# Kernel optimization log

Measured on AMD Instinct MI355X. Metric: run time of the kernel, lower is better.

The kernel has to match this reference:

```python
import jax, jax.numpy as jnp
import numpy as np

B, S, D, H = 4, 2048, 1024, 16
HD = D // H  # head_dim = 64


def setup_inputs() -> dict:
    key = jax.random.key(0)
    ks = jax.random.split(key, 9)
    sc = 1.0 / np.sqrt(D)
    return {
        "x": jax.random.normal(ks[0], (B, S, D), dtype=jnp.float32),
        "Wq": jax.random.normal(ks[1], (D, D), dtype=jnp.float32) * sc,
        "bq": jnp.zeros((D,), dtype=jnp.float32),
        "Wk": jax.random.normal(ks[2], (D, D), dtype=jnp.float32) * sc,
        "bk": jnp.zeros((D,), dtype=jnp.float32),
        "Wv": jax.random.normal(ks[3], (D, D), dtype=jnp.float32) * sc,
        "bv": jnp.zeros((D,), dtype=jnp.float32),
        "Wo": jax.random.normal(ks[4], (D, D), dtype=jnp.float32) * sc,
        "bo": jnp.zeros((D,), dtype=jnp.float32),
    }


def reference(x, Wq, bq, Wk, bk, Wv, bv, Wo, bo):
    # QKV projections (torch Linear: x @ W.T + b), reshape to [B, H, S, HD]
    def proj(W, b):
        return (x @ W.T + b).reshape(B, S, H, HD).transpose(0, 2, 1, 3)

    Q, K, V = proj(Wq, bq), proj(Wk, bk), proj(Wv, bv)
    scores = jnp.einsum("bhqd,bhkd->bhqk", Q, K) / jnp.sqrt(jnp.float32(HD))
    attn = jax.nn.softmax(scores, axis=-1)  # dropout is identity at eval
    ctx = jnp.einsum("bhqk,bhkd->bhqd", attn, V)
    ctx = ctx.transpose(0, 2, 1, 3).reshape(B, S, D)
    out = ctx @ Wo.T + bo
    return out, attn
```

## Files before the change

kernel.cpp:

```cpp
#include <hip/hip_runtime.h>
#include <stdint.h>

#define Mm 8192
#define Dd 1024

typedef unsigned short u16;
typedef __attribute__((ext_vector_type(8))) short bf16x8;
typedef __attribute__((ext_vector_type(4))) float f32x4;
typedef __attribute__((ext_vector_type(4))) u16 u16x4;

__device__ __forceinline__ u16 f2bf(float f) {
  union { float f; uint32_t u; } c; c.f = f;
  uint32_t u = c.u;
  return (u16)((u + 0x7fffu + ((u >> 16) & 1u)) >> 16);
}

__device__ __forceinline__ float EXP2(float x) {
#if __has_builtin(__builtin_amdgcn_exp2f)
  return __builtin_amdgcn_exp2f(x);
#else
  return exp2f(x);
#endif
}

__device__ __forceinline__ float LOG2(float x) {
#if __has_builtin(__builtin_amdgcn_logf)
  return __builtin_amdgcn_logf(x);
#else
  return log2f(x);
#endif
}

__device__ __forceinline__ uint32_t cvtpk(float a, float b) {
  uint32_t r;
  asm("v_cvt_pk_bf16_f32 %0, %1, %2" : "=v"(r) : "v"(a), "v"(b));
  return r;
}

__device__ __forceinline__ void gll16(const void* g, void* l) {
  __builtin_amdgcn_global_load_lds((const __attribute__((address_space(1))) void*)g,
                                   (__attribute__((address_space(3))) void*)l, 16, 0, 0);
}

__global__ void cvt_all(const float* __restrict__ x, const float* __restrict__ wq,
                        const float* __restrict__ wk, const float* __restrict__ wv,
                        const float* __restrict__ wo, u16* __restrict__ out) {
  const int xn4 = 2097152, wn4 = 262144;
  const int total = xn4 + 4 * wn4;
  int i = blockIdx.x * blockDim.x + threadIdx.x;
  int stride = gridDim.x * blockDim.x;
  for (; i < total; i += stride) {
    const float* src; int off;
    if (i < xn4) { src = x; off = i; }
    else {
      int j = i - xn4; int wsel = j >> 18; off = j & (wn4 - 1);
      src = (wsel == 0) ? wq : (wsel == 1) ? wk : (wsel == 2) ? wv : wo;
    }
    float4 v = ((const float4*)src)[off];
    u16x4 o;
    o.x = f2bf(v.x); o.y = f2bf(v.y); o.z = f2bf(v.z); o.w = f2bf(v.w);
    ((u16x4*)out)[i] = o;
  }
}

template<int MODE>
__global__ __launch_bounds__(256) void gemm_bt(
    const u16* __restrict__ A, const u16* __restrict__ Bt,
    const float* __restrict__ bias, void* __restrict__ out,
    int M, int N, int K, float scale)
{
  __shared__ u16 As[128 * 32];
  __shared__ u16 Bs[128 * 32];
  int tiles_n = N >> 7;
  int nwg = (M >> 7) * tiles_n;
  int bid = blockIdx.x;
  { int q = nwg >> 3; bid = (bid & 7) * q + (bid >> 3); }
  int tm = bid / tiles_n, tn = bid % tiles_n;
  int tid = threadIdx.x;
  int wid = tid >> 6, lane = tid & 63;
  int wr = wid >> 1, wc = wid & 1;

  f32x4 acc[4][4] = {};

  int a_row = wr * 64 + (lane & 15);
  int b_row = wc * 64 + (lane & 15);
  int frag_k = (lane >> 4) * 8;

  const u16* ga0 = A + (size_t)(tm * 128 + wid * 32 + (lane >> 2)) * K + (lane & 3) * 8;
  const u16* ga1 = ga0 + (size_t)16 * K;
  const u16* gb0 = Bt + (size_t)(tn * 128 + wid * 32 + (lane >> 2)) * K + (lane & 3) * 8;
  const u16* gb1 = gb0 + (size_t)16 * K;
  u16* lA0 = As + wid * 1024;
  u16* lA1 = As + wid * 1024 + 512;
  u16* lB0 = Bs + wid * 1024;
  u16* lB1 = Bs + wid * 1024 + 512;

  for (int kt = 0; kt < K; kt += 32) {
    gll16(ga0 + kt, lA0);
    gll16(ga1 + kt, lA1);
    gll16(gb0 + kt, lB0);
    gll16(gb1 + kt, lB1);
    __syncthreads();
    bf16x8 af[4], bfr[4];
#pragma unroll
    for (int i = 0; i < 4; i++)
      af[i] = *(const bf16x8*)(As + (a_row + i * 16) * 32 + frag_k);
#pragma unroll
    for (int i = 0; i < 4; i++)
      bfr[i] = *(const bf16x8*)(Bs + (b_row + i * 16) * 32 + frag_k);
#pragma unroll
    for (int i = 0; i < 4; i++)
#pragma unroll
      for (int j = 0; j < 4; j++)
        acc[i][j] = __builtin_amdgcn_mfma_f32_16x16x32_bf16(af[i], bfr[j], acc[i][j], 0, 0, 0);
    __syncthreads();
  }

#pragma unroll
  for (int i = 0; i < 4; i++) {
#pragma unroll
    for (int j = 0; j < 4; j++) {
      int col = tn * 128 + wc * 64 + j * 16 + (lane & 15);
      float bv = bias ? bias[col] : 0.f;
      if (MODE == 2) {
        int row0 = tm * 128 + wr * 64 + i * 16 + (lane >> 4) * 4;
        int b_ = row0 >> 11, s0 = row0 & 2047, h = col >> 6, hd = col & 63;
        u16x4 o;
#pragma unroll
        for (int r = 0; r < 4; r++) o[r] = f2bf((acc[i][j][r] + bv) * scale);
        *(u16x4*)&((u16*)out)[((size_t)(b_ * 16 + h) * 64 + hd) * 2048 + s0] = o;
      } else {
#pragma unroll
        for (int r = 0; r < 4; r++) {
          int row = tm * 128 + wr * 64 + i * 16 + (lane >> 4) * 4 + r;
          float v = (acc[i][j][r] + bv) * scale;
          if (MODE == 0) {
            int b_ = row >> 11, s = row & 2047, h = col >> 6, hd = col & 63;
            ((u16*)out)[(((size_t)(b_ * 16 + h) * 2048 + s) << 6) + hd] = f2bf(v);
          } else {
            ((float*)out)[(size_t)row * N + col] = v;
          }
        }
      }
    }
  }
}

__global__ __launch_bounds__(512) void attn_fused(
    const u16* __restrict__ Qb, const u16* __restrict__ Kb,
    const u16* __restrict__ Vtb, float* __restrict__ attn_out,
    u16* __restrict__ ctxb)
{
  __shared__ u16 Ks[4][4096];
  __shared__ u16 Vs[4][4096];
  __shared__ u16 Ps[8192];

  int bid = blockIdx.x;
  int swz = (bid & 7) * 128 + (bid >> 3);
  int bh = swz >> 4, qt = swz & 15;
  int tid = threadIdx.x, w = tid >> 6, lane = tid & 63;
  int g = lane >> 4, l15 = lane & 15;

  const u16* Qg = Qb + ((size_t)bh * 2048 + qt * 128) * 64;
  const u16* Kg = Kb + (size_t)bh * 2048 * 64;
  const u16* Vg = Vtb + (size_t)bh * 64 * 2048;
  float* Ag = attn_out + ((size_t)bh * 2048 + qt * 128) * 2048;

  int qloc = w * 16 + l15;
  bf16x8 aq0 = *(const bf16x8*)(Qg + (size_t)qloc * 64 + g * 8);
  bf16x8 aq1 = *(const bf16x8*)(Qg + (size_t)qloc * 64 + 32 + g * 8);

  int srow = w * 8 + (lane >> 3);
  int schunk = (lane & 7) ^ (lane >> 3);
  const u16* Ksrc = Kg + (size_t)srow * 64 + schunk * 8;
  const u16* Vsrc = Vg + (size_t)srow * 2048 + schunk * 8;

  float ls0 = 0.f, ls1 = 0.f, ls2 = 0.f, ls3 = 0.f;
#pragma unroll
  for (int p = 0; p < 3; p++)
    gll16(Ksrc + (size_t)p * 4096, (char*)Ks[p] + w * 1024);
  for (int it = 0; it < 32; ++it) {
    gll16(Ksrc + (size_t)((it + 3) & 31) * 4096, (char*)Ks[(it + 3) & 3] + w * 1024);
    asm volatile("s_waitcnt vmcnt(3)" ::: "memory");
    __builtin_amdgcn_s_barrier();
    f32x4 s[4] = {};
    const char* Kbase = (const char*)Ks[it & 3];
    __builtin_amdgcn_s_setprio(1);
#pragma unroll
    for (int t = 0; t < 4; t++) {
      int kr = t * 16 + l15;
      int x = (kr & 7) << 4;
      bf16x8 k0 = *(const bf16x8*)(Kbase + kr * 128 + ((g * 16) ^ x));
      bf16x8 k1 = *(const bf16x8*)(Kbase + kr * 128 + ((64 + g * 16) ^ x));
      s[t] = __builtin_amdgcn_mfma_f32_16x16x32_bf16(k0, aq0, s[t], 0, 0, 0);
      s[t] = __builtin_amdgcn_mfma_f32_16x16x32_bf16(k1, aq1, s[t], 0, 0, 0);
    }
    __builtin_amdgcn_s_setprio(0);
#pragma unroll
    for (int r = 0; r < 4; r++) {
      ls0 += EXP2(s[0][r]); ls1 += EXP2(s[1][r]);
      ls2 += EXP2(s[2][r]); ls3 += EXP2(s[3][r]);
    }
    asm volatile("" ::: "memory");
    __builtin_amdgcn_s_barrier();
  }
  float lsum = (ls0 + ls1) + (ls2 + ls3);
  lsum += __shfl_xor(lsum, 16);
  lsum += __shfl_xor(lsum, 32);
  float lr2 = -LOG2(lsum);

  f32x4 ctx[4] = {};
  int xq = (qloc & 7) << 4;
  char* Pb = (char*)Ps + qloc * 128;
#pragma unroll
  for (int p = 0; p < 3; p++) {
    gll16(Ksrc + (size_t)p * 4096, (char*)Ks[p] + w * 1024);
    gll16(Vsrc + (size_t)p * 64,  (char*)Vs[p] + w * 1024);
  }
  for (int it = 0; it < 32; ++it) {
    int nx = (it + 3) & 31;
    gll16(Ksrc + (size_t)nx * 4096, (char*)Ks[(it + 3) & 3] + w * 1024);
    gll16(Vsrc + (size_t)nx * 64,  (char*)Vs[(it + 3) & 3] + w * 1024);
    if (it == 0)      asm volatile("s_waitcnt vmcnt(6)" ::: "memory");
    else if (it == 1) asm volatile("s_waitcnt vmcnt(10)" ::: "memory");
    else if (it == 2) asm volatile("s_waitcnt vmcnt(14)" ::: "memory");
    else              asm volatile("s_waitcnt vmcnt(18)" ::: "memory");
    __builtin_amdgcn_s_barrier();
    f32x4 s[4] = {};
    const char* Kbase = (const char*)Ks[it & 3];
    __builtin_amdgcn_s_setprio(1);
#pragma unroll
    for (int t = 0; t < 4; t++) {
      int kr = t * 16 + l15;
      int x = (kr & 7) << 4;
      bf16x8 k0 = *(const bf16x8*)(Kbase + kr * 128 + ((g * 16) ^ x));
      bf16x8 k1 = *(const bf16x8*)(Kbase + kr * 128 + ((64 + g * 16) ^ x));
      s[t] = __builtin_amdgcn_mfma_f32_16x16x32_bf16(k0, aq0, s[t], 0, 0, 0);
      s[t] = __builtin_amdgcn_mfma_f32_16x16x32_bf16(k1, aq1, s[t], 0, 0, 0);
    }
    __builtin_amdgcn_s_setprio(0);
    float* Arow = Ag + (size_t)qloc * 2048 + it * 64 + g * 4;
#pragma unroll
    for (int t = 0; t < 4; t++) {
      f32x4 p;
#pragma unroll
      for (int r = 0; r < 4; r++) p[r] = EXP2(s[t][r] + lr2);
      __builtin_nontemporal_store(p, (f32x4*)(Arow + t * 16));
      uint2 pk;
      pk.x = cvtpk(p[0], p[1]);
      pk.y = cvtpk(p[2], p[3]);
      *(uint2*)(Pb + ((t * 32 + g * 8) ^ xq)) = pk;
    }
    __builtin_amdgcn_s_setprio(1);
#pragma unroll
    for (int kk = 0; kk < 2; kk++) {
      bf16x8 ap = *(const bf16x8*)(Pb + ((kk * 64 + g * 16) ^ xq));
#pragma unroll
      for (int t = 0; t < 4; t++) {
        int dr = t * 16 + l15;
        bf16x8 bv = *(const bf16x8*)((const char*)Vs[it & 3] + dr * 128 + ((kk * 64 + g * 16) ^ ((dr & 7) << 4)));
        ctx[t] = __builtin_amdgcn_mfma_f32_16x16x32_bf16(ap, bv, ctx[t], 0, 0, 0);
      }
    }
    __builtin_amdgcn_s_setprio(0);
    asm volatile("" ::: "memory");
    __builtin_amdgcn_s_barrier();
  }

  int b_ = bh >> 4, h = bh & 15;
#pragma unroll
  for (int t = 0; t < 4; t++)
#pragma unroll
    for (int r = 0; r < 4; r++) {
      int qg = qt * 128 + w * 16 + g * 4 + r;
      int col = h * 64 + t * 16 + l15;
      ctxb[((size_t)b_ * 2048 + qg) * 1024 + col] = f2bf(ctx[t][r]);
    }
}

extern "C" void kernel_launch(void* const* d_in, const int* in_sizes, int n_in,
                              void* d_out, int out_size, void* d_ws, size_t ws_size,
                              hipStream_t stream) {
  const float* x  = (const float*)d_in[0];
  const float* Wq = (const float*)d_in[1];
  const float* bq = (const float*)d_in[2];
  const float* Wk = (const float*)d_in[3];
  const float* bk = (const float*)d_in[4];
  const float* Wv = (const float*)d_in[5];
  const float* bv = (const float*)d_in[6];
  const float* Wo = (const float*)d_in[7];
  const float* bo = (const float*)d_in[8];

  u16* xb   = (u16*)d_ws;
  u16* Wqb  = xb + (size_t)Mm * Dd;
  u16* Wkb  = Wqb + (size_t)Dd * Dd;
  u16* Wvb  = Wkb + (size_t)Dd * Dd;
  u16* Wob  = Wvb + (size_t)Dd * Dd;
  u16* Qb   = Wob + (size_t)Dd * Dd;
  u16* Kbuf = Qb + (size_t)Mm * Dd;
  u16* Vtb  = Kbuf + (size_t)Mm * Dd;
  u16* ctxb = Vtb + (size_t)Mm * Dd;

  float* out_f = (float*)d_out;
  float* attn_o = out_f + (size_t)Mm * Dd;

  cvt_all<<<2048, 256, 0, stream>>>(x, Wq, Wk, Wv, Wo, xb);

  const float qscale = 0.125f * 1.44269504088896340736f;
  gemm_bt<0><<<512, 256, 0, stream>>>(xb, Wqb, bq, Qb,   Mm, Dd, Dd, qscale);
  gemm_bt<0><<<512, 256, 0, stream>>>(xb, Wkb, bk, Kbuf, Mm, Dd, Dd, 1.0f);
  gemm_bt<2><<<512, 256, 0, stream>>>(xb, Wvb, bv, Vtb,  Mm, Dd, Dd, 1.0f);
  attn_fused<<<1024, 512, 0, stream>>>(Qb, Kbuf, Vtb, attn_o, ctxb);
  gemm_bt<1><<<512, 256, 0, stream>>>(ctxb, Wob, bo, (void*)out_f, Mm, Dd, Dd, 1.0f);
}
```

Before: 453.9 us.

## Fuse QKV projections into one GEMM and process two query tiles per attention block

The three Q/K/V projection GEMMs become one launch over a concatenated N=3072 weight (Wq/Wk/Wv are contiguous in the workspace), with the epilogue routing columns to Q, K or transposed V. The attention kernel now handles two 128-row query tiles per block. The second tile's row-sum pass is folded into the first tile's output pass, so K tiles are reused and the standalone K sweep count drops from four to three. This trades fewer launches and less K traffic for a smaller grid (512 blocks), more registers, and hand-tuned vmcnt waits that risk being wrong.

New measurement: 532.0 us. 1.17x slower.

```diff
diff --git a/kernel.cpp b/kernel.cpp
--- a/kernel.cpp
+++ b/kernel.cpp
@@ -63,11 +63,87 @@
   }
 }
 
-template<int MODE>
-__global__ __launch_bounds__(256) void gemm_bt(
+__global__ __launch_bounds__(256) void gemm_qkv(
+    const u16* __restrict__ A, const u16* __restrict__ Wt,
+    const float* __restrict__ bq, const float* __restrict__ bk, const float* __restrict__ bv,
+    u16* __restrict__ Qo, u16* __restrict__ Ko, u16* __restrict__ Vo, float qscale)
+{
+  __shared__ u16 As[128 * 32];
+  __shared__ u16 Bs[128 * 32];
+  const int K = 1024, tiles_n = 24;
+  int nwg = 64 * 24;
+  int bid = blockIdx.x;
+  { int q = nwg >> 3; bid = (bid & 7) * q + (bid >> 3); }
+  int tm = bid / tiles_n, tn = bid % tiles_n;
+  int tid = threadIdx.x;
+  int wid = tid >> 6, lane = tid & 63;
+  int wr = wid >> 1, wc = wid & 1;
+
+  f32x4 acc[4][4] = {};
+  int a_row = wr * 64 + (lane & 15);
+  int b_row = wc * 64 + (lane & 15);
+  int frag_k = (lane >> 4) * 8;
+
+  const u16* ga0 = A + (size_t)(tm * 128 + wid * 32 + (lane >> 2)) * K + (lane & 3) * 8;
+  const u16* ga1 = ga0 + (size_t)16 * K;
+  const u16* gb0 = Wt + (size_t)(tn * 128 + wid * 32 + (lane >> 2)) * K + (lane & 3) * 8;
+  const u16* gb1 = gb0 + (size_t)16 * K;
+  u16* lA0 = As + wid * 1024;
+  u16* lA1 = As + wid * 1024 + 512;
+  u16* lB0 = Bs + wid * 1024;
+  u16* lB1 = Bs + wid * 1024 + 512;
+
+  for (int kt = 0; kt < K; kt += 32) {
+    gll16(ga0 + kt, lA0);
+    gll16(ga1 + kt, lA1);
+    gll16(gb0 + kt, lB0);
+    gll16(gb1 + kt, lB1);
+    __syncthreads();
+    bf16x8 af[4], bfr[4];
+#pragma unroll
+    for (int i = 0; i < 4; i++)
+      af[i] = *(const bf16x8*)(As + (a_row + i * 16) * 32 + frag_k);
+#pragma unroll
+    for (int i = 0; i < 4; i++)
+      bfr[i] = *(const bf16x8*)(Bs + (b_row + i * 16) * 32 + frag_k);
+#pragma unroll
+    for (int i = 0; i < 4; i++)
+#pragma unroll
+      for (int j = 0; j < 4; j++)
+        acc[i][j] = __builtin_amdgcn_mfma_f32_16x16x32_bf16(af[i], bfr[j], acc[i][j], 0, 0, 0);
+    __syncthreads();
+  }
+
+#pragma unroll
+  for (int i = 0; i < 4; i++) {
+#pragma unroll
+    for (int j = 0; j < 4; j++) {
+      int col = tn * 128 + wc * 64 + j * 16 + (lane & 15);
+      int wsel = col >> 10, c10 = col & 1023;
+      int h = c10 >> 6, hd = c10 & 63;
+      float bvv = (wsel == 0 ? bq : wsel == 1 ? bk : bv)[c10];
+      int row0 = tm * 128 + wr * 64 + i * 16 + (lane >> 4) * 4;
+      int b_ = row0 >> 11, s0 = row0 & 2047;
+      if (wsel == 2) {
+        u16x4 o;
+#pragma unroll
+        for (int r = 0; r < 4; r++) o[r] = f2bf(acc[i][j][r] + bvv);
+        *(u16x4*)&Vo[((size_t)(b_ * 16 + h) * 64 + hd) * 2048 + s0] = o;
+      } else {
+        u16* dst = (wsel == 0) ? Qo : Ko;
+        float sc = (wsel == 0) ? qscale : 1.0f;
+#pragma unroll
+        for (int r = 0; r < 4; r++)
+          dst[(((size_t)(b_ * 16 + h) * 2048 + (s0 + r)) << 6) + hd] = f2bf((acc[i][j][r] + bvv) * sc);
+      }
+    }
+  }
+}
+
+__global__ __launch_bounds__(256) void gemm_out(
     const u16* __restrict__ A, const u16* __restrict__ Bt,
-    const float* __restrict__ bias, void* __restrict__ out,
-    int M, int N, int K, float scale)
+    const float* __restrict__ bias, float* __restrict__ out,
+    int M, int N, int K)
 {
   __shared__ u16 As[128 * 32];
   __shared__ u16 Bs[128 * 32];
@@ -81,7 +157,6 @@
   int wr = wid >> 1, wc = wid & 1;
 
   f32x4 acc[4][4] = {};
-
   int a_row = wr * 64 + (lane & 15);
   int b_row = wc * 64 + (lane & 15);
   int frag_k = (lane >> 4) * 8;
@@ -117,36 +192,20 @@
   }
 
 #pragma unroll
-  for (int i = 0; i < 4; i++) {
+  for (int i = 0; i < 4; i++)
 #pragma unroll
     for (int j = 0; j < 4; j++) {
       int col = tn * 128 + wc * 64 + j * 16 + (lane & 15);
-      float bv = bias ? bias[col] : 0.f;
-      if (MODE == 2) {
-        int row0 = tm * 128 + wr * 64 + i * 16 + (lane >> 4) * 4;
-        int b_ = row0 >> 11, s0 = row0 & 2047, h = col >> 6, hd = col & 63;
-        u16x4 o;
-#pragma unroll
-        for (int r = 0; r < 4; r++) o[r] = f2bf((acc[i][j][r] + bv) * scale);
-        *(u16x4*)&((u16*)out)[((size_t)(b_ * 16 + h) * 64 + hd) * 2048 + s0] = o;
-      } else {
-#pragma unroll
-        for (int r = 0; r < 4; r++) {
-          int row = tm * 128 + wr * 64 + i * 16 + (lane >> 4) * 4 + r;
-          float v = (acc[i][j][r] + bv) * scale;
-          if (MODE == 0) {
-            int b_ = row >> 11, s = row & 2047, h = col >> 6, hd = col & 63;
-            ((u16*)out)[(((size_t)(b_ * 16 + h) * 2048 + s) << 6) + hd] = f2bf(v);
-          } else {
-            ((float*)out)[(size_t)row * N + col] = v;
-          }
-        }
+      float bv = bias[col];
+#pragma unroll
+      for (int r = 0; r < 4; r++) {
+        int row = tm * 128 + wr * 64 + i * 16 + (lane >> 4) * 4 + r;
+        out[(size_t)row * N + col] = acc[i][j][r] + bv;
       }
     }
-  }
-}
-
-__global__ __launch_bounds__(512) void attn_fused(
+}
+
+__global__ __launch_bounds__(512, 4) void attn_fused2(
     const u16* __restrict__ Qb, const u16* __restrict__ Kb,
     const u16* __restrict__ Vtb, float* __restrict__ attn_out,
     u16* __restrict__ ctxb)
@@ -156,32 +215,43 @@
   __shared__ u16 Ps[8192];
 
   int bid = blockIdx.x;
-  int swz = (bid & 7) * 128 + (bid >> 3);
-  int bh = swz >> 4, qt = swz & 15;
+  int swz = (bid & 7) * 64 + (bid >> 3);
+  int bh = swz >> 3, qtb = swz & 7;
   int tid = threadIdx.x, w = tid >> 6, lane = tid & 63;
   int g = lane >> 4, l15 = lane & 15;
 
-  const u16* Qg = Qb + ((size_t)bh * 2048 + qt * 128) * 64;
   const u16* Kg = Kb + (size_t)bh * 2048 * 64;
   const u16* Vg = Vtb + (size_t)bh * 64 * 2048;
-  float* Ag = attn_out + ((size_t)bh * 2048 + qt * 128) * 2048;
+  const u16* Qg0 = Qb + ((size_t)bh * 2048 + qtb * 256) * 64;
+  const u16* Qg1 = Qg0 + (size_t)128 * 64;
+  float* Ag0 = attn_out + ((size_t)bh * 2048 + qtb * 256) * 2048;
+  float* Ag1 = Ag0 + (size_t)128 * 2048;
 
   int qloc = w * 16 + l15;
-  bf16x8 aq0 = *(const bf16x8*)(Qg + (size_t)qloc * 64 + g * 8);
-  bf16x8 aq1 = *(const bf16x8*)(Qg + (size_t)qloc * 64 + 32 + g * 8);
+  bf16x8 aqA0 = *(const bf16x8*)(Qg0 + (size_t)qloc * 64 + g * 8);
+  bf16x8 aqA1 = *(const bf16x8*)(Qg0 + (size_t)qloc * 64 + 32 + g * 8);
+  bf16x8 aqB0 = *(const bf16x8*)(Qg1 + (size_t)qloc * 64 + g * 8);
+  bf16x8 aqB1 = *(const bf16x8*)(Qg1 + (size_t)qloc * 64 + 32 + g * 8);
 
   int srow = w * 8 + (lane >> 3);
   int schunk = (lane & 7) ^ (lane >> 3);
   const u16* Ksrc = Kg + (size_t)srow * 64 + schunk * 8;
   const u16* Vsrc = Vg + (size_t)srow * 2048 + schunk * 8;
 
+  int xq = (qloc & 7) << 4;
+  char* Pb = (char*)Ps + qloc * 128;
+  int b_ = bh >> 4, h = bh & 15;
+
   float ls0 = 0.f, ls1 = 0.f, ls2 = 0.f, ls3 = 0.f;
 #pragma unroll
   for (int p = 0; p < 3; p++)
     gll16(Ksrc + (size_t)p * 4096, (char*)Ks[p] + w * 1024);
   for (int it = 0; it < 32; ++it) {
-    gll16(Ksrc + (size_t)((it + 3) & 31) * 4096, (char*)Ks[(it + 3) & 3] + w * 1024);
-    asm volatile("s_waitcnt vmcnt(3)" ::: "memory");
+    if (it < 29) gll16(Ksrc + (size_t)(it + 3) * 4096, (char*)Ks[(it + 3) & 3] + w * 1024);
+    if (it < 29)      asm volatile("s_waitcnt vmcnt(3)" ::: "memory");
+    else if (it == 29) asm volatile("s_waitcnt vmcnt(2)" ::: "memory");
+    else if (it == 30) asm volatile("s_waitcnt vmcnt(1)" ::: "memory");
+    else               asm volatile("s_waitcnt vmcnt(0)" ::: "memory");
     __builtin_amdgcn_s_barrier();
     f32x4 s[4] = {};
     const char* Kbase = (const char*)Ks[it & 3];
@@ -192,8 +262,8 @@
       int x = (kr & 7) << 4;
       bf16x8 k0 = *(const bf16x8*)(Kbase + kr * 128 + ((g * 16) ^ x));
       bf16x8 k1 = *(const bf16x8*)(Kbase + kr * 128 + ((64 + g * 16) ^ x));
-      s[t] = __builtin_amdgcn_mfma_f32_16x16x32_bf16(k0, aq0, s[t], 0, 0, 0);
-      s[t] = __builtin_amdgcn_mfma_f32_16x16x32_bf16(k1, aq1, s[t], 0, 0, 0);
+      s[t] = __builtin_amdgcn_mfma_f32_16x16x32_bf16(k0, aqA0, s[t], 0, 0, 0);
+      s[t] = __builtin_amdgcn_mfma_f32_16x16x32_bf16(k1, aqA1, s[t], 0, 0, 0);
     }
     __builtin_amdgcn_s_setprio(0);
 #pragma unroll
@@ -207,24 +277,27 @@
   float lsum = (ls0 + ls1) + (ls2 + ls3);
   lsum += __shfl_xor(lsum, 16);
   lsum += __shfl_xor(lsum, 32);
-  float lr2 = -LOG2(lsum);
+  float lrA = -LOG2(lsum);
 
   f32x4 ctx[4] = {};
-  int xq = (qloc & 7) << 4;
-  char* Pb = (char*)Ps + qloc * 128;
+  float lb0 = 0.f, lb1 = 0.f, lb2 = 0.f, lb3 = 0.f;
+  asm volatile("s_waitcnt vmcnt(0)" ::: "memory");
+  __builtin_amdgcn_s_barrier();
 #pragma unroll
   for (int p = 0; p < 3; p++) {
     gll16(Ksrc + (size_t)p * 4096, (char*)Ks[p] + w * 1024);
     gll16(Vsrc + (size_t)p * 64,  (char*)Vs[p] + w * 1024);
   }
   for (int it = 0; it < 32; ++it) {
-    int nx = (it + 3) & 31;
-    gll16(Ksrc + (size_t)nx * 4096, (char*)Ks[(it + 3) & 3] + w * 1024);
-    gll16(Vsrc + (size_t)nx * 64,  (char*)Vs[(it + 3) & 3] + w * 1024);
+    if (it < 29) {
+      gll16(Ksrc + (size_t)(it + 3) * 4096, (char*)Ks[(it + 3) & 3] + w * 1024);
+      gll16(Vsrc + (size_t)(it + 3) * 64,  (char*)Vs[(it + 3) & 3] + w * 1024);
+    }
     if (it == 0)      asm volatile("s_waitcnt vmcnt(6)" ::: "memory");
-    else if (it == 1) asm volatile("s_waitcnt vmcnt(10)" ::: "memory");
-    else if (it == 2) asm volatile("s_waitcnt vmcnt(14)" ::: "memory");
-    else              asm volatile("s_waitcnt vmcnt(18)" ::: "memory");
+    else if (it == 1) asm volatile("s_waitcnt vmcnt(22)" ::: "memory");
+    else if (it == 2) asm volatile("s_waitcnt vmcnt(38)" ::: "memory");
+    else if (it < 29) asm volatile("s_waitcnt vmcnt(54)" ::: "memory");
+    else              asm volatile("s_waitcnt vmcnt(32)" ::: "memory");
     __builtin_amdgcn_s_barrier();
     f32x4 s[4] = {};
     const char* Kbase = (const char*)Ks[it & 3];
@@ -235,16 +308,16 @@
       int x = (kr & 7) << 4;
       bf16x8 k0 = *(const bf16x8*)(Kbase + kr * 128 + ((g * 16) ^ x));
       bf16x8 k1 = *(const bf16x8*)(Kbase + kr * 128 + ((64 + g * 16) ^ x));
-      s[t] = __builtin_amdgcn_mfma_f32_16x16x32_bf16(k0, aq0, s[t], 0, 0, 0);
-      s[t] = __builtin_amdgcn_mfma_f32_16x16x32_bf16(k1, aq1, s[t], 0, 0, 0);
+      s[t] = __builtin_amdgcn_mfma_f32_16x16x32_bf16(k0, aqA0, s[t], 0, 0, 0);
+      s[t] = __builtin_amdgcn_mfma_f32_16x16x32_bf16(k1, aqA1, s[t], 0, 0, 0);
     }
     __builtin_amdgcn_s_setprio(0);
-    float* Arow = Ag + (size_t)qloc * 2048 + it * 64 + g * 4;
+    float* Arow = Ag0 + (size_t)qloc * 2048 + it * 64 + g * 4;
 #pragma unroll
     for (int t = 0; t < 4; t++) {
       f32x4 p;
 #pragma unroll
-      for (int r = 0; r < 4; r++) p[r] = EXP2(s[t][r] + lr2);
+      for (int r = 0; r < 4; r++) p[r] = EXP2(s[t][r] + lrA);
       __builtin_nontemporal_store(p, (f32x4*)(Arow + t * 16));
       uint2 pk;
       pk.x = cvtpk(p[0], p[1]);
@@ -262,19 +335,106 @@
         ctx[t] = __builtin_amdgcn_mfma_f32_16x16x32_bf16(ap, bv, ctx[t], 0, 0, 0);
       }
     }
+    f32x4 sb[4] = {};
+#pragma unroll
+    for (int t = 0; t < 4; t++) {
+      int kr = t * 16 + l15;
+      int x = (kr & 7) << 4;
+      bf16x8 k0 = *(const bf16x8*)(Kbase + kr * 128 + ((g * 16) ^ x));
+      bf16x8 k1 = *(const bf16x8*)(Kbase + kr * 128 + ((64 + g * 16) ^ x));
+      sb[t] = __builtin_amdgcn_mfma_f32_16x16x32_bf16(k0, aqB0, sb[t], 0, 0, 0);
+      sb[t] = __builtin_amdgcn_mfma_f32_16x16x32_bf16(k1, aqB1, sb[t], 0, 0, 0);
+    }
+    __builtin_amdgcn_s_setprio(0);
+#pragma unroll
+    for (int r = 0; r < 4; r++) {
+      lb0 += EXP2(sb[0][r]); lb1 += EXP2(sb[1][r]);
+      lb2 += EXP2(sb[2][r]); lb3 += EXP2(sb[3][r]);
+    }
+    asm volatile("" ::: "memory");
+    __builtin_amdgcn_s_barrier();
+  }
+  float lsb = (lb0 + lb1) + (lb2 + lb3);
+  lsb += __shfl_xor(lsb, 16);
+  lsb += __shfl_xor(lsb, 32);
+  float lrB = -LOG2(lsb);
+
+#pragma unroll
+  for (int t = 0; t < 4; t++)
+#pragma unroll
+    for (int r = 0; r < 4; r++) {
+      int qg = qtb * 256 + w * 16 + g * 4 + r;
+      int col = h * 64 + t * 16 + l15;
+      ctxb[((size_t)b_ * 2048 + qg) * 1024 + col] = f2bf(ctx[t][r]);
+    }
+
+  f32x4 ctxB[4] = {};
+  asm volatile("s_waitcnt vmcnt(0)" ::: "memory");
+  __builtin_amdgcn_s_barrier();
+#pragma unroll
+  for (int p = 0; p < 3; p++) {
+    gll16(Ksrc + (size_t)p * 4096, (char*)Ks[p] + w * 1024);
+    gll16(Vsrc + (size_t)p * 64,  (char*)Vs[p] + w * 1024);
+  }
+  for (int it = 0; it < 32; ++it) {
+    if (it < 29) {
+      gll16(Ksrc + (size_t)(it + 3) * 4096, (char*)Ks[(it + 3) & 3] + w * 1024);
+      gll16(Vsrc + (size_t)(it + 3) * 64,  (char*)Vs[(it + 3) & 3] + w * 1024);
+    }
+    if (it == 0)      asm volatile("s_waitcnt vmcnt(6)" ::: "memory");
+    else if (it == 1) asm volatile("s_waitcnt vmcnt(22)" ::: "memory");
+    else if (it == 2) asm volatile("s_waitcnt vmcnt(38)" ::: "memory");
+    else if (it < 29) asm volatile("s_waitcnt vmcnt(54)" ::: "memory");
+    else              asm volatile("s_waitcnt vmcnt(32)" ::: "memory");
+    __builtin_amdgcn_s_barrier();
+    f32x4 s[4] = {};
+    const char* Kbase = (const char*)Ks[it & 3];
+    __builtin_amdgcn_s_setprio(1);
+#pragma unroll
+    for (int t = 0; t < 4; t++) {
+      int kr = t * 16 + l15;
+      int x = (kr & 7) << 4;
+      bf16x8 k0 = *(const bf16x8*)(Kbase + kr * 128 + ((g * 16) ^ x));
+      bf16x8 k1 = *(const bf16x8*)(Kbase + kr * 128 + ((64 + g * 16) ^ x));
+      s[t] = __builtin_amdgcn_mfma_f32_16x16x32_bf16(k0, aqB0, s[t], 0, 0, 0);
+      s[t] = __builtin_amdgcn_mfma_f32_16x16x32_bf16(k1, aqB1, s[t], 0, 0, 0);
+    }
+    __builtin_amdgcn_s_setprio(0);
+    float* Arow = Ag1 + (size_t)qloc * 2048 + it * 64 + g * 4;
+#pragma unroll
+    for (int t = 0; t < 4; t++) {
+      f32x4 p;
+#pragma unroll
+      for (int r = 0; r < 4; r++) p[r] = EXP2(s[t][r] + lrB);
+      __builtin_nontemporal_store(p, (f32x4*)(Arow + t * 16));
+      uint2 pk;
+      pk.x = cvtpk(p[0], p[1]);
+      pk.y = cvtpk(p[2], p[3]);
+      *(uint2*)(Pb + ((t * 32 + g * 8) ^ xq)) = pk;
+    }
+    __builtin_amdgcn_s_setprio(1);
+#pragma unroll
+    for (int kk = 0; kk < 2; kk++) {
+      bf16x8 ap = *(const bf16x8*)(Pb + ((kk * 64 + g * 16) ^ xq));
+#pragma unroll
+      for (int t = 0; t < 4; t++) {
+        int dr = t * 16 + l15;
+        bf16x8 bv = *(const bf16x8*)((const char*)Vs[it & 3] + dr * 128 + ((kk * 64 + g * 16) ^ ((dr & 7) << 4)));
+        ctxB[t] = __builtin_amdgcn_mfma_f32_16x16x32_bf16(ap, bv, ctxB[t], 0, 0, 0);
+      }
+    }
     __builtin_amdgcn_s_setprio(0);
     asm volatile("" ::: "memory");
     __builtin_amdgcn_s_barrier();
   }
 
-  int b_ = bh >> 4, h = bh & 15;
 #pragma unroll
   for (int t = 0; t < 4; t++)
 #pragma unroll
     for (int r = 0; r < 4; r++) {
-      int qg = qt * 128 + w * 16 + g * 4 + r;
+      int qg = qtb * 256 + 128 + w * 16 + g * 4 + r;
       int col = h * 64 + t * 16 + l15;
-      ctxb[((size_t)b_ * 2048 + qg) * 1024 + col] = f2bf(ctx[t][r]);
+      ctxb[((size_t)b_ * 2048 + qg) * 1024 + col] = f2bf(ctxB[t][r]);
     }
 }
 
@@ -307,9 +467,7 @@
   cvt_all<<<2048, 256, 0, stream>>>(x, Wq, Wk, Wv, Wo, xb);
 
   const float qscale = 0.125f * 1.44269504088896340736f;
-  gemm_bt<0><<<512, 256, 0, stream>>>(xb, Wqb, bq, Qb,   Mm, Dd, Dd, qscale);
-  gemm_bt<0><<<512, 256, 0, stream>>>(xb, Wkb, bk, Kbuf, Mm, Dd, Dd, 1.0f);
-  gemm_bt<2><<<512, 256, 0, stream>>>(xb, Wvb, bv, Vtb,  Mm, Dd, Dd, 1.0f);
-  attn_fused<<<1024, 512, 0, stream>>>(Qb, Kbuf, Vtb, attn_o, ctxb);
-  gemm_bt<1><<<512, 256, 0, stream>>>(ctxb, Wob, bo, (void*)out_f, Mm, Dd, Dd, 1.0f);
-}
+  gemm_qkv<<<1536, 256, 0, stream>>>(xb, Wqb, bq, bk, bv, Qb, Kbuf, Vtb, qscale);
+  attn_fused2<<<512, 512, 0, stream>>>(Qb, Kbuf, Vtb, attn_o, ctxb);
+  gemm_out<<<512, 256, 0, stream>>>(ctxb, Wob, bo, out_f, Mm, Dd, Dd);
+}
```
